# Kernel optimization log

Hardware: AMD Instinct MI355X
Metric: run time of the kernel (lower is better)

## Reference

```python
import jax, jax.numpy as jnp
import numpy as np

N_NODES = 20000
N_EDGES = 40000
MAX_NB = 6
N_ATOM_FEAT = 98
N_BOND_FEAT = 13
HIDDEN = 256
DEPTH = 4
INPUT_SIZE = N_ATOM_FEAT + N_BOND_FEAT  # 111, hmess width


def setup_inputs() -> dict:
    key = jax.random.key(0)
    ks = jax.random.split(key, 10)
    fnode = jax.random.normal(ks[0], (N_NODES, N_ATOM_FEAT), jnp.float32)
    # fmess: col0/col1 are src/dst node indices stored as floats, cols 2: are bond features
    idx = jax.random.randint(ks[1], (N_EDGES, 2), 0, N_NODES).astype(jnp.float32)
    bond = jax.random.normal(ks[2], (N_EDGES, N_BOND_FEAT), jnp.float32)
    fmess = jnp.concatenate([idx, bond], axis=1)  # [E, 2 + n_bond_feat]
    agraph = jax.random.randint(ks[3], (N_NODES, MAX_NB), 0, N_EDGES)
    bgraph = jax.random.randint(ks[4], (N_EDGES, MAX_NB), 0, N_EDGES)
    s = 0.02
    W_z_w = jax.random.normal(ks[5], (HIDDEN, INPUT_SIZE + HIDDEN), jnp.float32) * s
    W_z_b = jnp.zeros((HIDDEN,), jnp.float32)
    W_r_w = jax.random.normal(ks[6], (HIDDEN, INPUT_SIZE), jnp.float32) * s  # no bias (W_r)
    U_r_w = jax.random.normal(ks[7], (HIDDEN, HIDDEN), jnp.float32) * s
    U_r_b = jnp.zeros((HIDDEN,), jnp.float32)
    W_h_w = jax.random.normal(ks[8], (HIDDEN, INPUT_SIZE + HIDDEN), jnp.float32) * s
    W_h_b = jnp.zeros((HIDDEN,), jnp.float32)
    W_o_w = jax.random.normal(ks[9], (HIDDEN, N_ATOM_FEAT + HIDDEN), jnp.float32) * s
    W_o_b = jnp.zeros((HIDDEN,), jnp.float32)
    return dict(fnode=fnode, fmess=fmess, agraph=agraph, bgraph=bgraph,
                W_z_w=W_z_w, W_z_b=W_z_b, W_r_w=W_r_w, U_r_w=U_r_w, U_r_b=U_r_b,
                W_h_w=W_h_w, W_h_b=W_h_b, W_o_w=W_o_w, W_o_b=W_o_b)


def reference(fnode, fmess, agraph, bgraph,
              W_z_w, W_z_b, W_r_w, U_r_w, U_r_b, W_h_w, W_h_b, W_o_w, W_o_b):
    # GraphFeatEncoder: gather src-node features and concat with bond features
    src = fmess[:, 0].astype(jnp.int32)
    x = jnp.concatenate([fnode[src], fmess[:, 2:]], axis=-1)  # [E, input_size]
    E = x.shape[0]
    H = W_z_b.shape[0]
    emask = jnp.ones((E, 1), x.dtype).at[0, 0].set(0.0)  # message 0 is padding
    Wr_x = (x @ W_r_w.T)[:, None, :]  # [E,1,H], constant across depth iterations
    h = jnp.zeros((E, H), x.dtype)
    # DGCNGRU: D-MPNN style GRU over directed-edge states
    for _ in range(DEPTH):
        h_nei = h[bgraph]                                   # [E, max_nb, H] gather
        sum_h = h_nei.sum(axis=1)                           # [E, H]
        z = jax.nn.sigmoid(jnp.concatenate([x, sum_h], axis=1) @ W_z_w.T + W_z_b)
        r = jax.nn.sigmoid(Wr_x + h_nei @ U_r_w.T + U_r_b)  # [E, max_nb, H]
        sum_gh = (r * h_nei).sum(axis=1)
        pre_h = jnp.tanh(jnp.concatenate([x, sum_gh], axis=1) @ W_h_w.T + W_h_b)
        h = ((1.0 - z) * sum_h + z * pre_h) * emask
    # DGCNEncoder readout: aggregate incoming edge states per atom
    nei_msg = h[agraph].sum(axis=1)                          # [N, H] gather + sum
    node_h = jax.nn.gelu(jnp.concatenate([fnode, nei_msg], axis=1) @ W_o_w.T + W_o_b,
                         approximate=False)                  # torch nn.GELU = exact erf
    nmask = jnp.ones((node_h.shape[0], 1), node_h.dtype).at[0, 0].set(0.0)  # node 0 pad
    hatom = node_h * nmask
    return hatom  # GraphFeatEncoder returns (hatom, None); hmol is always None
```

## Files before the change

kernel.cpp:

```cpp
#include <hip/hip_runtime.h>
#include <cstddef>
#include <cstdint>

typedef unsigned short u16;
typedef unsigned int   u32;
typedef __bf16  bf16x8 __attribute__((ext_vector_type(8)));
typedef float   f32x4  __attribute__((ext_vector_type(4)));

#define DEV __device__ __forceinline__

DEV float b2f(u16 u) { union { u32 i; float f; } c; c.i = ((u32)u) << 16; return c.f; }
DEV u16 f2b(float x) { union { float f; u32 i; } c; c.f = x; u32 b = c.i;
                       return (u16)((b + 0x7FFFu + ((b >> 16) & 1u)) >> 16); }
DEV float sigm(float x)  { return 1.0f / (1.0f + __expf(-x)); }
DEV float tanh_(float x) { return 1.0f - 2.0f / (1.0f + __expf(2.0f * x)); }
DEV float gelu_(float x) { return 0.5f * x * (1.0f + erff(x * 0.70710678118654752f)); }

DEV void u4tof8(uint4 v, float* f) {
    f[0] = b2f((u16)(v.x & 0xFFFF)); f[1] = b2f((u16)(v.x >> 16));
    f[2] = b2f((u16)(v.y & 0xFFFF)); f[3] = b2f((u16)(v.y >> 16));
    f[4] = b2f((u16)(v.z & 0xFFFF)); f[5] = b2f((u16)(v.z >> 16));
    f[6] = b2f((u16)(v.w & 0xFFFF)); f[7] = b2f((u16)(v.w >> 16));
}
DEV uint4 f8tou4(const float* f) {
    uint4 v;
    v.x = (u32)f2b(f[0]) | ((u32)f2b(f[1]) << 16);
    v.y = (u32)f2b(f[2]) | ((u32)f2b(f[3]) << 16);
    v.z = (u32)f2b(f[4]) | ((u32)f2b(f[5]) << 16);
    v.w = (u32)f2b(f[6]) | ((u32)f2b(f[7]) << 16);
    return v;
}

#define OB_X     0ull
#define OB_FB    10240000ull
#define OB_PRU   15360000ull
#define OB_H     35840000ull
#define OB_UH    56320000ull
#define OB_SH    76800000ull
#define OB_SGH   97280000ull
#define OB_BZ    117760000ull
#define OB_BH    117956608ull
#define OB_BU    118153216ull
#define OB_BR    118284288ull
#define OB_BO    118349824ull
#define WS_BYTES 118546432ull


__global__ __launch_bounds__(256) void k_repack(
    const float* __restrict__ Wz, const float* __restrict__ Wr,
    const float* __restrict__ Ur, const float* __restrict__ Wh,
    const float* __restrict__ Wo,
    u16* __restrict__ BzT, u16* __restrict__ BhT, u16* __restrict__ BuT,
    u16* __restrict__ BrT, u16* __restrict__ BoT) {
    int idx = blockIdx.x * 256 + threadIdx.x;
    {
        int n = idx / 384, k = idx % 384;
        float vz, vh, vo;
        if (k < 111)      { vz = Wz[n * 367 + k];      vh = Wh[n * 367 + k]; }
        else if (k < 128) { vz = 0.0f;                 vh = 0.0f; }
        else              { vz = Wz[n * 367 + k - 17]; vh = Wh[n * 367 + k - 17]; }
        if (k < 98)       vo = Wo[n * 354 + k];
        else if (k < 128) vo = 0.0f;
        else              vo = Wo[n * 354 + k - 30];
        BzT[idx] = f2b(vz); BhT[idx] = f2b(vh); BoT[idx] = f2b(vo);
    }
    if (idx < 65536) BuT[idx] = f2b(Ur[idx]);
    if (idx < 32768) {
        int n = idx >> 7, k = idx & 127;
        BrT[idx] = f2b(k < 111 ? Wr[n * 111 + k] : 0.0f);
    }
}

__global__ __launch_bounds__(256) void k_build_x(const float* __restrict__ fnode,
                                                 const float* __restrict__ fmess,
                                                 u16* __restrict__ x) {
    int e = (blockIdx.x << 1) + (threadIdx.x >> 7);
    int c = threadIdx.x & 127;
    int src = (int)fmess[(size_t)e * 15];
    float v = 0.0f;
    if (c < 98)       v = fnode[(size_t)src * 98 + c];
    else if (c < 111) v = fmess[(size_t)e * 15 + 2 + (c - 98)];
    x[(size_t)e * 128 + c] = f2b(v);
}

__global__ __launch_bounds__(256) void k_build_fb(const float* __restrict__ fnode,
                                                  u16* __restrict__ fb) {
    int idx = blockIdx.x * 256 + threadIdx.x;
    int n = idx >> 7, c = idx & 127;
    fb[idx] = f2b(c < 98 ? fnode[(size_t)n * 98 + c] : 0.0f);
}

DEV void ldA(const u16* __restrict__ g, size_t row0, int ld, int k0, int tid, uint4* v) {
    #pragma unroll
    for (int it = 0; it < 4; ++it) {
        int r = it * 32 + (tid >> 3);
        int c = (tid & 7) << 3;
        v[it] = *(const uint4*)(g + (row0 + (size_t)r) * ld + k0 + c);
    }
}
DEV void ldB(const u16* __restrict__ g, size_t row0, int ld, int k0, int tid, uint4* v) {
    #pragma unroll
    for (int it = 0; it < 2; ++it) {
        int r = it * 32 + (tid >> 3);
        int c = (tid & 7) << 3;
        v[it] = *(const uint4*)(g + (row0 + (size_t)r) * ld + k0 + c);
    }
}
DEV void wrA(u16* s, int tid, const uint4* v) {
    #pragma unroll
    for (int it = 0; it < 4; ++it) {
        int r = it * 32 + (tid >> 3);
        int c = (tid & 7) << 3;
        int byte = (((r << 6) + c) << 1) ^ ((r & 7) << 4);
        *(uint4*)((char*)s + byte) = v[it];
    }
}
DEV void wrB(u16* s, int tid, const uint4* v) {
    #pragma unroll
    for (int it = 0; it < 2; ++it) {
        int r = it * 32 + (tid >> 3);
        int c = (tid & 7) << 3;
        int byte = (((r << 6) + c) << 1) ^ ((r & 7) << 4);
        *(uint4*)((char*)s + byte) = v[it];
    }
}
DEV void mma_step(const u16* As, const u16* Bs, f32x4 acc[4][2], int lane, int wr, int wc) {
    int rb = (wr << 6) + (lane & 15);
    int cb = (wc << 5) + (lane & 15);
    int ko = (lane >> 4) << 3;
    #pragma unroll
    for (int kh = 0; kh < 2; ++kh) {
        bf16x8 a[4], b[2];
        #pragma unroll
        for (int i = 0; i < 4; ++i) {
            int ar = rb + (i << 4);
            a[i] = *(const bf16x8*)((const char*)As +
                   ((((ar << 6) + (kh << 5) + ko) << 1) ^ ((ar & 7) << 4)));
        }
        #pragma unroll
        for (int j = 0; j < 2; ++j) {
            int br = cb + (j << 4);
            b[j] = *(const bf16x8*)((const char*)Bs +
                   ((((br << 6) + (kh << 5) + ko) << 1) ^ ((br & 7) << 4)));
        }
        #pragma unroll
        for (int i = 0; i < 4; ++i)
            #pragma unroll
            for (int j = 0; j < 2; ++j)
                acc[i][j] = __builtin_amdgcn_mfma_f32_16x16x32_bf16(b[j], a[i], acc[i][j], 0, 0, 0);
    }
}

#define GT_PROLOG()                                            \
    int tid = threadIdx.x, lane = tid & 63, w = tid >> 6;      \
    int wr = w >> 1, wc = w & 1;                               \
    int bm = blockIdx.x >> 2, bn = blockIdx.x & 3;             \
    size_t m0 = (size_t)bm << 7; size_t n0 = (size_t)(bn << 6);\
    int row_l = (wr << 6) + (lane & 15);                       \
    int col_l = (wc << 5) + ((lane >> 4) << 2);

#define ACC_INIT(A)                                            \
    { f32x4 zz = {0.f, 0.f, 0.f, 0.f};                         \
      _Pragma("unroll") for (int i = 0; i < 4; ++i)            \
      _Pragma("unroll") for (int j = 0; j < 2; ++j) A[i][j] = zz; }

#define DB_STEP(CUR_A, CUR_B, NXT_A, NXT_B, LD_NEXT2)          \
    mma_step(CUR_A, CUR_B, acc, lane, wr, wc);                 \
    wrA(NXT_A, tid, ra); wrB(NXT_B, tid, rb);                  \
    __syncthreads();                                           \
    LD_NEXT2;

__global__ __launch_bounds__(256) void k_mg_z(
    const u16* __restrict__ x, const u16* __restrict__ sumh,
    const u16* __restrict__ BzT, const float* __restrict__ bz,
    u16* __restrict__ zb) {
    __shared__ u16 As0[8192], As1[8192], Bs0[4096], Bs1[4096];
    GT_PROLOG()
    f32x4 acc[4][2]; ACC_INIT(acc)
    uint4 ra[4], rb[2];
    ldA(x, m0, 128, 0, tid, ra); ldB(BzT, n0, 384, 0, tid, rb);
    wrA(As0, tid, ra); wrB(Bs0, tid, rb);
    __syncthreads();
    ldA(x, m0, 128, 64, tid, ra); ldB(BzT, n0, 384, 64, tid, rb);
    DB_STEP(As0, Bs0, As1, Bs1, (ldA(sumh, m0, 256, 0, tid, ra),   ldB(BzT, n0, 384, 128, tid, rb)))
    DB_STEP(As1, Bs1, As0, Bs0, (ldA(sumh, m0, 256, 64, tid, ra),  ldB(BzT, n0, 384, 192, tid, rb)))
    DB_STEP(As0, Bs0, As1, Bs1, (ldA(sumh, m0, 256, 128, tid, ra), ldB(BzT, n0, 384, 256, tid, rb)))
    DB_STEP(As1, Bs1, As0, Bs0, (ldA(sumh, m0, 256, 192, tid, ra), ldB(BzT, n0, 384, 320, tid, rb)))
    DB_STEP(As0, Bs0, As1, Bs1, ;)
    mma_step(As1, Bs1, acc, lane, wr, wc);
    #pragma unroll
    for (int mi = 0; mi < 4; ++mi) {
        int m = (int)m0 + row_l + (mi << 4);
        if (m >= 40000) continue;
        #pragma unroll
        for (int ni = 0; ni < 2; ++ni) {
            int col = (int)n0 + col_l + (ni << 4);
            float4 vz = *(const float4*)(bz + col);
            ushort4 o;
            o.x = f2b(sigm(acc[mi][ni][0] + vz.x));
            o.y = f2b(sigm(acc[mi][ni][1] + vz.y));
            o.z = f2b(sigm(acc[mi][ni][2] + vz.z));
            o.w = f2b(sigm(acc[mi][ni][3] + vz.w));
            *(ushort4*)(zb + (size_t)m * 256 + col) = o;
        }
    }
}

__global__ __launch_bounds__(256) void k_mg_h(
    const u16* __restrict__ x, const u16* __restrict__ sumgh,
    const u16* __restrict__ sumh, const u16* __restrict__ zb,
    const u16* __restrict__ BhT, const float* __restrict__ bh,
    u16* __restrict__ h) {
    __shared__ u16 As0[8192], As1[8192], Bs0[4096], Bs1[4096];
    GT_PROLOG()
    f32x4 acc[4][2]; ACC_INIT(acc)
    uint4 ra[4], rb[2];
    ldA(x, m0, 128, 0, tid, ra); ldB(BhT, n0, 384, 0, tid, rb);
    wrA(As0, tid, ra); wrB(Bs0, tid, rb);
    __syncthreads();
    ldA(x, m0, 128, 64, tid, ra); ldB(BhT, n0, 384, 64, tid, rb);
    DB_STEP(As0, Bs0, As1, Bs1, (ldA(sumgh, m0, 256, 0, tid, ra),   ldB(BhT, n0, 384, 128, tid, rb)))
    DB_STEP(As1, Bs1, As0, Bs0, (ldA(sumgh, m0, 256, 64, tid, ra),  ldB(BhT, n0, 384, 192, tid, rb)))
    DB_STEP(As0, Bs0, As1, Bs1, (ldA(sumgh, m0, 256, 128, tid, ra), ldB(BhT, n0, 384, 256, tid, rb)))
    DB_STEP(As1, Bs1, As0, Bs0, (ldA(sumgh, m0, 256, 192, tid, ra), ldB(BhT, n0, 384, 320, tid, rb)))
    DB_STEP(As0, Bs0, As1, Bs1, ;)
    mma_step(As1, Bs1, acc, lane, wr, wc);
    #pragma unroll
    for (int mi = 0; mi < 4; ++mi) {
        int m = (int)m0 + row_l + (mi << 4);
        if (m >= 40000) continue;
        #pragma unroll
        for (int ni = 0; ni < 2; ++ni) {
            int col = (int)n0 + col_l + (ni << 4);
            float4 vh = *(const float4*)(bh + col);
            ushort4 z4  = *(const ushort4*)(zb   + (size_t)m * 256 + col);
            ushort4 sh4 = *(const ushort4*)(sumh + (size_t)m * 256 + col);
            float zv[4]  = {b2f(z4.x),  b2f(z4.y),  b2f(z4.z),  b2f(z4.w)};
            float shv[4] = {b2f(sh4.x), b2f(sh4.y), b2f(sh4.z), b2f(sh4.w)};
            float bhv[4] = {vh.x, vh.y, vh.z, vh.w};
            float o[4];
            #pragma unroll
            for (int q = 0; q < 4; ++q) {
                float pre = tanh_(acc[mi][ni][q] + bhv[q]);
                o[q] = (1.0f - zv[q]) * shv[q] + zv[q] * pre;
            }
            if (m == 0) { o[0] = o[1] = o[2] = o[3] = 0.0f; }
            ushort4 ov;
            ov.x = f2b(o[0]); ov.y = f2b(o[1]); ov.z = f2b(o[2]); ov.w = f2b(o[3]);
            *(ushort4*)(h + (size_t)m * 256 + col) = ov;
        }
    }
}

__global__ __launch_bounds__(256) void k_d1z(
    const u16* __restrict__ x, const u16* __restrict__ BzT,
    const float* __restrict__ bz, u16* __restrict__ zb) {
    __shared__ u16 As0[8192], As1[8192], Bs0[4096], Bs1[4096];
    GT_PROLOG()
    f32x4 acc[4][2]; ACC_INIT(acc)
    uint4 ra[4], rb[2];
    ldA(x, m0, 128, 0, tid, ra); ldB(BzT, n0, 384, 0, tid, rb);
    wrA(As0, tid, ra); wrB(Bs0, tid, rb);
    __syncthreads();
    ldA(x, m0, 128, 64, tid, ra); ldB(BzT, n0, 384, 64, tid, rb);
    DB_STEP(As0, Bs0, As1, Bs1, ;)
    mma_step(As1, Bs1, acc, lane, wr, wc);
    #pragma unroll
    for (int mi = 0; mi < 4; ++mi) {
        int m = (int)m0 + row_l + (mi << 4);
        if (m >= 40000) continue;
        #pragma unroll
        for (int ni = 0; ni < 2; ++ni) {
            int col = (int)n0 + col_l + (ni << 4);
            float4 vz = *(const float4*)(bz + col);
            ushort4 o;
            o.x = f2b(sigm(acc[mi][ni][0] + vz.x));
            o.y = f2b(sigm(acc[mi][ni][1] + vz.y));
            o.z = f2b(sigm(acc[mi][ni][2] + vz.z));
            o.w = f2b(sigm(acc[mi][ni][3] + vz.w));
            *(ushort4*)(zb + (size_t)m * 256 + col) = o;
        }
    }
}

__global__ __launch_bounds__(256) void k_d1h(
    const u16* __restrict__ x, const u16* __restrict__ zb,
    const u16* __restrict__ BhT, const float* __restrict__ bh,
    u16* __restrict__ h) {
    __shared__ u16 As0[8192], As1[8192], Bs0[4096], Bs1[4096];
    GT_PROLOG()
    f32x4 acc[4][2]; ACC_INIT(acc)
    uint4 ra[4], rb[2];
    ldA(x, m0, 128, 0, tid, ra); ldB(BhT, n0, 384, 0, tid, rb);
    wrA(As0, tid, ra); wrB(Bs0, tid, rb);
    __syncthreads();
    ldA(x, m0, 128, 64, tid, ra); ldB(BhT, n0, 384, 64, tid, rb);
    DB_STEP(As0, Bs0, As1, Bs1, ;)
    mma_step(As1, Bs1, acc, lane, wr, wc);
    #pragma unroll
    for (int mi = 0; mi < 4; ++mi) {
        int m = (int)m0 + row_l + (mi << 4);
        if (m >= 40000) continue;
        #pragma unroll
        for (int ni = 0; ni < 2; ++ni) {
            int col = (int)n0 + col_l + (ni << 4);
            float4 vh = *(const float4*)(bh + col);
            ushort4 z4 = *(const ushort4*)(zb + (size_t)m * 256 + col);
            float zv[4] = {b2f(z4.x), b2f(z4.y), b2f(z4.z), b2f(z4.w)};
            float o[4];
            o[0] = zv[0] * tanh_(acc[mi][ni][0] + vh.x);
            o[1] = zv[1] * tanh_(acc[mi][ni][1] + vh.y);
            o[2] = zv[2] * tanh_(acc[mi][ni][2] + vh.z);
            o[3] = zv[3] * tanh_(acc[mi][ni][3] + vh.w);
            if (m == 0) { o[0] = o[1] = o[2] = o[3] = 0.0f; }
            ushort4 ov;
            ov.x = f2b(o[0]); ov.y = f2b(o[1]); ov.z = f2b(o[2]); ov.w = f2b(o[3]);
            *(ushort4*)(h + (size_t)m * 256 + col) = ov;
        }
    }
}

__global__ __launch_bounds__(256) void k_mg_uh(
    const u16* __restrict__ A, const u16* __restrict__ BT, u16* __restrict__ C) {
    __shared__ u16 As0[8192], As1[8192], Bs0[4096], Bs1[4096];
    GT_PROLOG()
    f32x4 acc[4][2]; ACC_INIT(acc)
    uint4 ra[4], rb[2];
    ldA(A, m0, 256, 0, tid, ra); ldB(BT, n0, 256, 0, tid, rb);
    wrA(As0, tid, ra); wrB(Bs0, tid, rb);
    __syncthreads();
    ldA(A, m0, 256, 64, tid, ra); ldB(BT, n0, 256, 64, tid, rb);
    DB_STEP(As0, Bs0, As1, Bs1, (ldA(A, m0, 256, 128, tid, ra), ldB(BT, n0, 256, 128, tid, rb)))
    DB_STEP(As1, Bs1, As0, Bs0, (ldA(A, m0, 256, 192, tid, ra), ldB(BT, n0, 256, 192, tid, rb)))
    DB_STEP(As0, Bs0, As1, Bs1, ;)
    mma_step(As1, Bs1, acc, lane, wr, wc);
    #pragma unroll
    for (int mi = 0; mi < 4; ++mi) {
        int m = (int)m0 + row_l + (mi << 4);
        if (m >= 40000) continue;
        #pragma unroll
        for (int ni = 0; ni < 2; ++ni) {
            int col = (int)n0 + col_l + (ni << 4);
            ushort4 o;
            o.x = f2b(acc[mi][ni][0]); o.y = f2b(acc[mi][ni][1]);
            o.z = f2b(acc[mi][ni][2]); o.w = f2b(acc[mi][ni][3]);
            *(ushort4*)(C + (size_t)m * 256 + col) = o;
        }
    }
}

__global__ __launch_bounds__(256) void k_mg_p(
    const u16* __restrict__ x, const u16* __restrict__ BrT,
    const float* __restrict__ urb, u16* __restrict__ PrU) {
    __shared__ u16 As0[8192], As1[8192], Bs0[4096], Bs1[4096];
    GT_PROLOG()
    f32x4 acc[4][2]; ACC_INIT(acc)
    uint4 ra[4], rb[2];
    ldA(x, m0, 128, 0, tid, ra); ldB(BrT, n0, 128, 0, tid, rb);
    wrA(As0, tid, ra); wrB(Bs0, tid, rb);
    __syncthreads();
    ldA(x, m0, 128, 64, tid, ra); ldB(BrT, n0, 128, 64, tid, rb);
    DB_STEP(As0, Bs0, As1, Bs1, ;)
    mma_step(As1, Bs1, acc, lane, wr, wc);
    #pragma unroll
    for (int mi = 0; mi < 4; ++mi) {
        int m = (int)m0 + row_l + (mi << 4);
        if (m >= 40000) continue;
        #pragma unroll
        for (int ni = 0; ni < 2; ++ni) {
            int col = (int)n0 + col_l + (ni << 4);
            float4 ub = *(const float4*)(urb + col);
            ushort4 o;
            o.x = f2b(acc[mi][ni][0] + ub.x); o.y = f2b(acc[mi][ni][1] + ub.y);
            o.z = f2b(acc[mi][ni][2] + ub.z); o.w = f2b(acc[mi][ni][3] + ub.w);
            *(ushort4*)(PrU + (size_t)m * 256 + col) = o;
        }
    }
}

__global__ __launch_bounds__(256) void k_mg_out(
    const u16* __restrict__ fb, const u16* __restrict__ nei,
    const u16* __restrict__ BoT, const float* __restrict__ bo,
    float* __restrict__ out) {
    __shared__ u16 As0[8192], As1[8192], Bs0[4096], Bs1[4096];
    GT_PROLOG()
    f32x4 acc[4][2]; ACC_INIT(acc)
    uint4 ra[4], rb[2];
    ldA(fb, m0, 128, 0, tid, ra); ldB(BoT, n0, 384, 0, tid, rb);
    wrA(As0, tid, ra); wrB(Bs0, tid, rb);
    __syncthreads();
    ldA(fb, m0, 128, 64, tid, ra); ldB(BoT, n0, 384, 64, tid, rb);
    DB_STEP(As0, Bs0, As1, Bs1, (ldA(nei, m0, 256, 0, tid, ra),   ldB(BoT, n0, 384, 128, tid, rb)))
    DB_STEP(As1, Bs1, As0, Bs0, (ldA(nei, m0, 256, 64, tid, ra),  ldB(BoT, n0, 384, 192, tid, rb)))
    DB_STEP(As0, Bs0, As1, Bs1, (ldA(nei, m0, 256, 128, tid, ra), ldB(BoT, n0, 384, 256, tid, rb)))
    DB_STEP(As1, Bs1, As0, Bs0, (ldA(nei, m0, 256, 192, tid, ra), ldB(BoT, n0, 384, 320, tid, rb)))
    DB_STEP(As0, Bs0, As1, Bs1, ;)
    mma_step(As1, Bs1, acc, lane, wr, wc);
    #pragma unroll
    for (int mi = 0; mi < 4; ++mi) {
        int m = (int)m0 + row_l + (mi << 4);
        if (m >= 20000) continue;
        #pragma unroll
        for (int ni = 0; ni < 2; ++ni) {
            int col = (int)n0 + col_l + (ni << 4);
            float4 vb = *(const float4*)(bo + col);
            float4 o;
            o.x = gelu_(acc[mi][ni][0] + vb.x);
            o.y = gelu_(acc[mi][ni][1] + vb.y);
            o.z = gelu_(acc[mi][ni][2] + vb.z);
            o.w = gelu_(acc[mi][ni][3] + vb.w);
            if (m == 0) { o.x = o.y = o.z = o.w = 0.0f; }
            *(float4*)(out + (size_t)m * 256 + col) = o;
        }
    }
}

__global__ __launch_bounds__(256) void k_gather_edge(
    const u16* __restrict__ h, const u16* __restrict__ Uh,
    const u16* __restrict__ PrU, const int* __restrict__ bgraph,
    u16* __restrict__ sumh, u16* __restrict__ sumgh) {
    int e = (blockIdx.x << 3) + (threadIdx.x >> 5);
    int c = (threadIdx.x & 31) << 3;
    size_t o = (size_t)e * 256 + c;
    float pr[8];
    u4tof8(*(const uint4*)(PrU + o), pr);
    float sh[8] = {}, sg[8] = {};
    #pragma unroll
    for (int j = 0; j < 6; ++j) {
        int b = bgraph[e * 6 + j];
        float hv[8], uv[8];
        u4tof8(*(const uint4*)(h  + (size_t)b * 256 + c), hv);
        u4tof8(*(const uint4*)(Uh + (size_t)b * 256 + c), uv);
        #pragma unroll
        for (int q = 0; q < 8; ++q) {
            sh[q] += hv[q];
            sg[q] += sigm(pr[q] + uv[q]) * hv[q];
        }
    }
    *(uint4*)(sumh  + o) = f8tou4(sh);
    *(uint4*)(sumgh + o) = f8tou4(sg);
}

__global__ __launch_bounds__(256) void k_gather_node(
    const u16* __restrict__ h, const int* __restrict__ agraph,
    u16* __restrict__ nei) {
    int n = (blockIdx.x << 3) + (threadIdx.x >> 5);
    int c = (threadIdx.x & 31) << 3;
    float s[8] = {};
    #pragma unroll
    for (int j = 0; j < 6; ++j) {
        int a = agraph[n * 6 + j];
        float hv[8];
        u4tof8(*(const uint4*)(h + (size_t)a * 256 + c), hv);
        #pragma unroll
        for (int q = 0; q < 8; ++q) s[q] += hv[q];
    }
    *(uint4*)(nei + (size_t)n * 256 + c) = f8tou4(s);
}

extern "C" void kernel_launch(void* const* d_in, const int* in_sizes, int n_in,
                              void* d_out, int out_size, void* d_ws, size_t ws_size,
                              hipStream_t stream) {
    if (ws_size < WS_BYTES) return;

    const float* fnode  = (const float*)d_in[0];
    const float* fmess  = (const float*)d_in[1];
    const int*   agraph = (const int*)d_in[2];
    const int*   bgraph = (const int*)d_in[3];
    const float* Wz  = (const float*)d_in[4];
    const float* bz  = (const float*)d_in[5];
    const float* Wr  = (const float*)d_in[6];
    const float* Ur  = (const float*)d_in[7];
    const float* urb = (const float*)d_in[8];
    const float* Wh  = (const float*)d_in[9];
    const float* bh  = (const float*)d_in[10];
    const float* Wo  = (const float*)d_in[11];
    const float* bo  = (const float*)d_in[12];

    char* base = (char*)d_ws;
    u16* x     = (u16*)(base + OB_X);
    u16* fb    = (u16*)(base + OB_FB);
    u16* PrU   = (u16*)(base + OB_PRU);
    u16* h     = (u16*)(base + OB_H);
    u16* Uh    = (u16*)(base + OB_UH);
    u16* zb    = (u16*)(base + OB_UH);
    u16* nei   = (u16*)(base + OB_UH);
    u16* sumh  = (u16*)(base + OB_SH);
    u16* sumgh = (u16*)(base + OB_SGH);
    u16* BzT   = (u16*)(base + OB_BZ);
    u16* BhT   = (u16*)(base + OB_BH);
    u16* BuT   = (u16*)(base + OB_BU);
    u16* BrT   = (u16*)(base + OB_BR);
    u16* BoT   = (u16*)(base + OB_BO);
    float* out = (float*)d_out;

    hipLaunchKernelGGL(k_repack, dim3(384), dim3(256), 0, stream,
                       Wz, Wr, Ur, Wh, Wo, BzT, BhT, BuT, BrT, BoT);
    hipLaunchKernelGGL(k_build_x, dim3(20000), dim3(256), 0, stream, fnode, fmess, x);
    hipLaunchKernelGGL(k_build_fb, dim3(10000), dim3(256), 0, stream, fnode, fb);
    hipLaunchKernelGGL(k_mg_p, dim3(1252), dim3(256), 0, stream, x, BrT, urb, PrU);
    hipLaunchKernelGGL(k_d1z, dim3(1252), dim3(256), 0, stream, x, BzT, bz, zb);
    hipLaunchKernelGGL(k_d1h, dim3(1252), dim3(256), 0, stream, x, zb, BhT, bh, h);
    for (int d = 1; d < 4; ++d) {
        hipLaunchKernelGGL(k_mg_uh, dim3(1252), dim3(256), 0, stream, h, BuT, Uh);
        hipLaunchKernelGGL(k_gather_edge, dim3(5000), dim3(256), 0, stream,
                           h, Uh, PrU, bgraph, sumh, sumgh);
        hipLaunchKernelGGL(k_mg_z, dim3(1252), dim3(256), 0, stream,
                           x, sumh, BzT, bz, zb);
        hipLaunchKernelGGL(k_mg_h, dim3(1252), dim3(256), 0, stream,
                           x, sumgh, sumh, zb, BhT, bh, h);
    }
    hipLaunchKernelGGL(k_gather_node, dim3(2500), dim3(256), 0, stream, h, agraph, nei);
    hipLaunchKernelGGL(k_mg_out, dim3(628), dim3(256), 0, stream, fb, nei, BoT, bo, out);
}
```

Before: 470.4 us.

## Precompute depth-invariant x projections and split GEMMs into x and hidden parts

The x-dependent parts of the z, h and output projections are computed once up front as Pzx, Phx and a partial output, so the per-depth z/h GEMMs only multiply the 256-wide hidden part (K drops from 384 to 256). The first depth becomes an elementwise kernel, and the output GEMM adds a precomputed fnode partial stored in out. Tiles are also remapped across XCDs, and the gather kernels prefetch their indices and neighbour rows one step ahead. This cuts repeated GEMM work per depth but adds extra bf16 intermediate buffers and rounding of the partial projections.

Result: faster. 444.1 us (-5.6%).

```diff
diff --git a/kernel.cpp b/kernel.cpp
--- a/kernel.cpp
+++ b/kernel.cpp
@@ -31,43 +31,51 @@
     return v;
 }
 
-#define OB_X     0ull
-#define OB_FB    10240000ull
-#define OB_PRU   15360000ull
-#define OB_H     35840000ull
-#define OB_UH    56320000ull
-#define OB_SH    76800000ull
-#define OB_SGH   97280000ull
-#define OB_BZ    117760000ull
-#define OB_BH    117956608ull
-#define OB_BU    118153216ull
-#define OB_BR    118284288ull
-#define OB_BO    118349824ull
-#define WS_BYTES 118546432ull
-
+#define OB_PRU   0ull
+#define OB_PZX   20480000ull
+#define OB_PHX   40960000ull
+#define OB_H     61440000ull
+#define OB_UH    81920000ull
+#define OB_SH    102400000ull
+#define OB_SGH   122880000ull
+#define OB_BZX   143360000ull
+#define OB_BZH   143425536ull
+#define OB_BHX   143556608ull
+#define OB_BHH   143622144ull
+#define OB_BU    143753216ull
+#define OB_BOH   143884288ull
+#define OB_BR    OB_UH
+#define OB_BOX   (OB_UH + 65536ull)
+#define WS_BYTES 144015360ull
+
+
+DEV int xcd_swz(int bid, int nwg) {
+    int q = nwg >> 3, r = nwg & 7;
+    int xcd = bid & 7, idx = bid >> 3;
+    return (xcd < r ? xcd * (q + 1) : r * (q + 1) + (xcd - r) * q) + idx;
+}
 
 __global__ __launch_bounds__(256) void k_repack(
     const float* __restrict__ Wz, const float* __restrict__ Wr,
     const float* __restrict__ Ur, const float* __restrict__ Wh,
     const float* __restrict__ Wo,
-    u16* __restrict__ BzT, u16* __restrict__ BhT, u16* __restrict__ BuT,
-    u16* __restrict__ BrT, u16* __restrict__ BoT) {
+    u16* __restrict__ BzxT, u16* __restrict__ BzhT, u16* __restrict__ BhxT,
+    u16* __restrict__ BhhT, u16* __restrict__ BuT, u16* __restrict__ BohT,
+    u16* __restrict__ BrT, u16* __restrict__ BoxT) {
     int idx = blockIdx.x * 256 + threadIdx.x;
     {
-        int n = idx / 384, k = idx % 384;
-        float vz, vh, vo;
-        if (k < 111)      { vz = Wz[n * 367 + k];      vh = Wh[n * 367 + k]; }
-        else if (k < 128) { vz = 0.0f;                 vh = 0.0f; }
-        else              { vz = Wz[n * 367 + k - 17]; vh = Wh[n * 367 + k - 17]; }
-        if (k < 98)       vo = Wo[n * 354 + k];
-        else if (k < 128) vo = 0.0f;
-        else              vo = Wo[n * 354 + k - 30];
-        BzT[idx] = f2b(vz); BhT[idx] = f2b(vh); BoT[idx] = f2b(vo);
-    }
-    if (idx < 65536) BuT[idx] = f2b(Ur[idx]);
+        int n = idx >> 8, k = idx & 255;
+        BzhT[idx] = f2b(Wz[n * 367 + 111 + k]);
+        BhhT[idx] = f2b(Wh[n * 367 + 111 + k]);
+        BuT[idx]  = f2b(Ur[idx]);
+        BohT[idx] = f2b(Wo[n * 354 + 98 + k]);
+    }
     if (idx < 32768) {
         int n = idx >> 7, k = idx & 127;
-        BrT[idx] = f2b(k < 111 ? Wr[n * 111 + k] : 0.0f);
+        BzxT[idx] = f2b(k < 111 ? Wz[n * 367 + k] : 0.0f);
+        BhxT[idx] = f2b(k < 111 ? Wh[n * 367 + k] : 0.0f);
+        BrT[idx]  = f2b(k < 111 ? Wr[n * 111 + k] : 0.0f);
+        BoxT[idx] = f2b(k < 98  ? Wo[n * 354 + k] : 0.0f);
     }
 }
 
@@ -154,7 +162,8 @@
 #define GT_PROLOG()                                            \
     int tid = threadIdx.x, lane = tid & 63, w = tid >> 6;      \
     int wr = w >> 1, wc = w & 1;                               \
-    int bm = blockIdx.x >> 2, bn = blockIdx.x & 3;             \
+    int bid = xcd_swz((int)blockIdx.x, (int)gridDim.x);        \
+    int bm = bid >> 2, bn = bid & 3;                           \
     size_t m0 = (size_t)bm << 7; size_t n0 = (size_t)(bn << 6);\
     int row_l = (wr << 6) + (lane & 15);                       \
     int col_l = (wc << 5) + ((lane >> 4) << 2);
@@ -170,22 +179,17 @@
     __syncthreads();                                           \
     LD_NEXT2;
 
-__global__ __launch_bounds__(256) void k_mg_z(
-    const u16* __restrict__ x, const u16* __restrict__ sumh,
-    const u16* __restrict__ BzT, const float* __restrict__ bz,
-    u16* __restrict__ zb) {
+__global__ __launch_bounds__(256) void k_mg_k128(
+    const u16* __restrict__ A, const u16* __restrict__ BT,
+    const float* __restrict__ bias, u16* __restrict__ out) {
     __shared__ u16 As0[8192], As1[8192], Bs0[4096], Bs1[4096];
     GT_PROLOG()
     f32x4 acc[4][2]; ACC_INIT(acc)
     uint4 ra[4], rb[2];
-    ldA(x, m0, 128, 0, tid, ra); ldB(BzT, n0, 384, 0, tid, rb);
+    ldA(A, m0, 128, 0, tid, ra); ldB(BT, n0, 128, 0, tid, rb);
     wrA(As0, tid, ra); wrB(Bs0, tid, rb);
     __syncthreads();
-    ldA(x, m0, 128, 64, tid, ra); ldB(BzT, n0, 384, 64, tid, rb);
-    DB_STEP(As0, Bs0, As1, Bs1, (ldA(sumh, m0, 256, 0, tid, ra),   ldB(BzT, n0, 384, 128, tid, rb)))
-    DB_STEP(As1, Bs1, As0, Bs0, (ldA(sumh, m0, 256, 64, tid, ra),  ldB(BzT, n0, 384, 192, tid, rb)))
-    DB_STEP(As0, Bs0, As1, Bs1, (ldA(sumh, m0, 256, 128, tid, ra), ldB(BzT, n0, 384, 256, tid, rb)))
-    DB_STEP(As1, Bs1, As0, Bs0, (ldA(sumh, m0, 256, 192, tid, ra), ldB(BzT, n0, 384, 320, tid, rb)))
+    ldA(A, m0, 128, 64, tid, ra); ldB(BT, n0, 128, 64, tid, rb);
     DB_STEP(As0, Bs0, As1, Bs1, ;)
     mma_step(As1, Bs1, acc, lane, wr, wc);
     #pragma unroll
@@ -195,129 +199,57 @@
         #pragma unroll
         for (int ni = 0; ni < 2; ++ni) {
             int col = (int)n0 + col_l + (ni << 4);
-            float4 vz = *(const float4*)(bz + col);
+            float4 ub = bias ? *(const float4*)(bias + col)
+                             : make_float4(0.f, 0.f, 0.f, 0.f);
             ushort4 o;
-            o.x = f2b(sigm(acc[mi][ni][0] + vz.x));
-            o.y = f2b(sigm(acc[mi][ni][1] + vz.y));
-            o.z = f2b(sigm(acc[mi][ni][2] + vz.z));
-            o.w = f2b(sigm(acc[mi][ni][3] + vz.w));
-            *(ushort4*)(zb + (size_t)m * 256 + col) = o;
-        }
-    }
-}
-
-__global__ __launch_bounds__(256) void k_mg_h(
-    const u16* __restrict__ x, const u16* __restrict__ sumgh,
-    const u16* __restrict__ sumh, const u16* __restrict__ zb,
-    const u16* __restrict__ BhT, const float* __restrict__ bh,
-    u16* __restrict__ h) {
+            o.x = f2b(acc[mi][ni][0] + ub.x); o.y = f2b(acc[mi][ni][1] + ub.y);
+            o.z = f2b(acc[mi][ni][2] + ub.z); o.w = f2b(acc[mi][ni][3] + ub.w);
+            *(ushort4*)(out + (size_t)m * 256 + col) = o;
+        }
+    }
+}
+
+__global__ __launch_bounds__(256) void k_mg_pn(
+    const u16* __restrict__ fb, const u16* __restrict__ BT,
+    float* __restrict__ out) {
     __shared__ u16 As0[8192], As1[8192], Bs0[4096], Bs1[4096];
     GT_PROLOG()
     f32x4 acc[4][2]; ACC_INIT(acc)
     uint4 ra[4], rb[2];
-    ldA(x, m0, 128, 0, tid, ra); ldB(BhT, n0, 384, 0, tid, rb);
+    ldA(fb, m0, 128, 0, tid, ra); ldB(BT, n0, 128, 0, tid, rb);
     wrA(As0, tid, ra); wrB(Bs0, tid, rb);
     __syncthreads();
-    ldA(x, m0, 128, 64, tid, ra); ldB(BhT, n0, 384, 64, tid, rb);
-    DB_STEP(As0, Bs0, As1, Bs1, (ldA(sumgh, m0, 256, 0, tid, ra),   ldB(BhT, n0, 384, 128, tid, rb)))
-    DB_STEP(As1, Bs1, As0, Bs0, (ldA(sumgh, m0, 256, 64, tid, ra),  ldB(BhT, n0, 384, 192, tid, rb)))
-    DB_STEP(As0, Bs0, As1, Bs1, (ldA(sumgh, m0, 256, 128, tid, ra), ldB(BhT, n0, 384, 256, tid, rb)))
-    DB_STEP(As1, Bs1, As0, Bs0, (ldA(sumgh, m0, 256, 192, tid, ra), ldB(BhT, n0, 384, 320, tid, rb)))
+    ldA(fb, m0, 128, 64, tid, ra); ldB(BT, n0, 128, 64, tid, rb);
     DB_STEP(As0, Bs0, As1, Bs1, ;)
     mma_step(As1, Bs1, acc, lane, wr, wc);
     #pragma unroll
     for (int mi = 0; mi < 4; ++mi) {
         int m = (int)m0 + row_l + (mi << 4);
-        if (m >= 40000) continue;
+        if (m >= 20000) continue;
         #pragma unroll
         for (int ni = 0; ni < 2; ++ni) {
             int col = (int)n0 + col_l + (ni << 4);
-            float4 vh = *(const float4*)(bh + col);
-            ushort4 z4  = *(const ushort4*)(zb   + (size_t)m * 256 + col);
-            ushort4 sh4 = *(const ushort4*)(sumh + (size_t)m * 256 + col);
-            float zv[4]  = {b2f(z4.x),  b2f(z4.y),  b2f(z4.z),  b2f(z4.w)};
-            float shv[4] = {b2f(sh4.x), b2f(sh4.y), b2f(sh4.z), b2f(sh4.w)};
-            float bhv[4] = {vh.x, vh.y, vh.z, vh.w};
-            float o[4];
             #pragma unroll
-            for (int q = 0; q < 4; ++q) {
-                float pre = tanh_(acc[mi][ni][q] + bhv[q]);
-                o[q] = (1.0f - zv[q]) * shv[q] + zv[q] * pre;
-            }
-            if (m == 0) { o[0] = o[1] = o[2] = o[3] = 0.0f; }
-            ushort4 ov;
-            ov.x = f2b(o[0]); ov.y = f2b(o[1]); ov.z = f2b(o[2]); ov.w = f2b(o[3]);
-            *(ushort4*)(h + (size_t)m * 256 + col) = ov;
-        }
-    }
-}
-
-__global__ __launch_bounds__(256) void k_d1z(
-    const u16* __restrict__ x, const u16* __restrict__ BzT,
-    const float* __restrict__ bz, u16* __restrict__ zb) {
-    __shared__ u16 As0[8192], As1[8192], Bs0[4096], Bs1[4096];
-    GT_PROLOG()
-    f32x4 acc[4][2]; ACC_INIT(acc)
-    uint4 ra[4], rb[2];
-    ldA(x, m0, 128, 0, tid, ra); ldB(BzT, n0, 384, 0, tid, rb);
-    wrA(As0, tid, ra); wrB(Bs0, tid, rb);
-    __syncthreads();
-    ldA(x, m0, 128, 64, tid, ra); ldB(BzT, n0, 384, 64, tid, rb);
-    DB_STEP(As0, Bs0, As1, Bs1, ;)
-    mma_step(As1, Bs1, acc, lane, wr, wc);
-    #pragma unroll
-    for (int mi = 0; mi < 4; ++mi) {
-        int m = (int)m0 + row_l + (mi << 4);
-        if (m >= 40000) continue;
-        #pragma unroll
-        for (int ni = 0; ni < 2; ++ni) {
-            int col = (int)n0 + col_l + (ni << 4);
-            float4 vz = *(const float4*)(bz + col);
-            ushort4 o;
-            o.x = f2b(sigm(acc[mi][ni][0] + vz.x));
-            o.y = f2b(sigm(acc[mi][ni][1] + vz.y));
-            o.z = f2b(sigm(acc[mi][ni][2] + vz.z));
-            o.w = f2b(sigm(acc[mi][ni][3] + vz.w));
-            *(ushort4*)(zb + (size_t)m * 256 + col) = o;
-        }
-    }
-}
-
-__global__ __launch_bounds__(256) void k_d1h(
-    const u16* __restrict__ x, const u16* __restrict__ zb,
-    const u16* __restrict__ BhT, const float* __restrict__ bh,
+            for (int q = 0; q < 4; ++q)
+                out[(size_t)m * 256 + col + q] = acc[mi][ni][q];
+        }
+    }
+}
+
+__global__ __launch_bounds__(256) void k_d1(
+    const u16* __restrict__ Pzx, const u16* __restrict__ Phx,
+    const float* __restrict__ bz, const float* __restrict__ bh,
     u16* __restrict__ h) {
-    __shared__ u16 As0[8192], As1[8192], Bs0[4096], Bs1[4096];
-    GT_PROLOG()
-    f32x4 acc[4][2]; ACC_INIT(acc)
-    uint4 ra[4], rb[2];
-    ldA(x, m0, 128, 0, tid, ra); ldB(BhT, n0, 384, 0, tid, rb);
-    wrA(As0, tid, ra); wrB(Bs0, tid, rb);
-    __syncthreads();
-    ldA(x, m0, 128, 64, tid, ra); ldB(BhT, n0, 384, 64, tid, rb);
-    DB_STEP(As0, Bs0, As1, Bs1, ;)
-    mma_step(As1, Bs1, acc, lane, wr, wc);
-    #pragma unroll
-    for (int mi = 0; mi < 4; ++mi) {
-        int m = (int)m0 + row_l + (mi << 4);
-        if (m >= 40000) continue;
-        #pragma unroll
-        for (int ni = 0; ni < 2; ++ni) {
-            int col = (int)n0 + col_l + (ni << 4);
-            float4 vh = *(const float4*)(bh + col);
-            ushort4 z4 = *(const ushort4*)(zb + (size_t)m * 256 + col);
-            float zv[4] = {b2f(z4.x), b2f(z4.y), b2f(z4.z), b2f(z4.w)};
-            float o[4];
-            o[0] = zv[0] * tanh_(acc[mi][ni][0] + vh.x);
-            o[1] = zv[1] * tanh_(acc[mi][ni][1] + vh.y);
-            o[2] = zv[2] * tanh_(acc[mi][ni][2] + vh.z);
-            o[3] = zv[3] * tanh_(acc[mi][ni][3] + vh.w);
-            if (m == 0) { o[0] = o[1] = o[2] = o[3] = 0.0f; }
-            ushort4 ov;
-            ov.x = f2b(o[0]); ov.y = f2b(o[1]); ov.z = f2b(o[2]); ov.w = f2b(o[3]);
-            *(ushort4*)(h + (size_t)m * 256 + col) = ov;
-        }
-    }
+    int idx = blockIdx.x * 256 + threadIdx.x;
+    int e = idx >> 5, c = (idx & 31) << 3;
+    size_t o = (size_t)e * 256 + c;
+    float pz[8], ph[8], r[8];
+    u4tof8(*(const uint4*)(Pzx + o), pz);
+    u4tof8(*(const uint4*)(Phx + o), ph);
+    #pragma unroll
+    for (int q = 0; q < 8; ++q)
+        r[q] = (e == 0) ? 0.0f : sigm(pz[q] + bz[c + q]) * tanh_(ph[q] + bh[c + q]);
+    *(uint4*)(h + o) = f8tou4(r);
 }
 
 __global__ __launch_bounds__(256) void k_mg_uh(
@@ -349,17 +281,20 @@
     }
 }
 
-__global__ __launch_bounds__(256) void k_mg_p(
-    const u16* __restrict__ x, const u16* __restrict__ BrT,
-    const float* __restrict__ urb, u16* __restrict__ PrU) {
+__global__ __launch_bounds__(256) void k_mg_z(
+    const u16* __restrict__ sumh, const u16* __restrict__ BT,
+    const u16* __restrict__ Pzx, const float* __restrict__ bz,
+    u16* __restrict__ zb) {
     __shared__ u16 As0[8192], As1[8192], Bs0[4096], Bs1[4096];
     GT_PROLOG()
     f32x4 acc[4][2]; ACC_INIT(acc)
     uint4 ra[4], rb[2];
-    ldA(x, m0, 128, 0, tid, ra); ldB(BrT, n0, 128, 0, tid, rb);
+    ldA(sumh, m0, 256, 0, tid, ra); ldB(BT, n0, 256, 0, tid, rb);
     wrA(As0, tid, ra); wrB(Bs0, tid, rb);
     __syncthreads();
-    ldA(x, m0, 128, 64, tid, ra); ldB(BrT, n0, 128, 64, tid, rb);
+    ldA(sumh, m0, 256, 64, tid, ra); ldB(BT, n0, 256, 64, tid, rb);
+    DB_STEP(As0, Bs0, As1, Bs1, (ldA(sumh, m0, 256, 128, tid, ra), ldB(BT, n0, 256, 128, tid, rb)))
+    DB_STEP(As1, Bs1, As0, Bs0, (ldA(sumh, m0, 256, 192, tid, ra), ldB(BT, n0, 256, 192, tid, rb)))
     DB_STEP(As0, Bs0, As1, Bs1, ;)
     mma_step(As1, Bs1, acc, lane, wr, wc);
     #pragma unroll
@@ -369,31 +304,77 @@
         #pragma unroll
         for (int ni = 0; ni < 2; ++ni) {
             int col = (int)n0 + col_l + (ni << 4);
-            float4 ub = *(const float4*)(urb + col);
+            float4 vz = *(const float4*)(bz + col);
+            ushort4 p4 = *(const ushort4*)(Pzx + (size_t)m * 256 + col);
             ushort4 o;
-            o.x = f2b(acc[mi][ni][0] + ub.x); o.y = f2b(acc[mi][ni][1] + ub.y);
-            o.z = f2b(acc[mi][ni][2] + ub.z); o.w = f2b(acc[mi][ni][3] + ub.w);
-            *(ushort4*)(PrU + (size_t)m * 256 + col) = o;
-        }
-    }
-}
-
-__global__ __launch_bounds__(256) void k_mg_out(
-    const u16* __restrict__ fb, const u16* __restrict__ nei,
-    const u16* __restrict__ BoT, const float* __restrict__ bo,
-    float* __restrict__ out) {
+            o.x = f2b(sigm(acc[mi][ni][0] + b2f(p4.x) + vz.x));
+            o.y = f2b(sigm(acc[mi][ni][1] + b2f(p4.y) + vz.y));
+            o.z = f2b(sigm(acc[mi][ni][2] + b2f(p4.z) + vz.z));
+            o.w = f2b(sigm(acc[mi][ni][3] + b2f(p4.w) + vz.w));
+            *(ushort4*)(zb + (size_t)m * 256 + col) = o;
+        }
+    }
+}
+
+__global__ __launch_bounds__(256) void k_mg_h(
+    const u16* __restrict__ sumgh, const u16* __restrict__ BT,
+    const u16* __restrict__ Phx, const float* __restrict__ bh,
+    const u16* __restrict__ zb, const u16* __restrict__ sumh,
+    u16* __restrict__ h) {
     __shared__ u16 As0[8192], As1[8192], Bs0[4096], Bs1[4096];
     GT_PROLOG()
     f32x4 acc[4][2]; ACC_INIT(acc)
     uint4 ra[4], rb[2];
-    ldA(fb, m0, 128, 0, tid, ra); ldB(BoT, n0, 384, 0, tid, rb);
+    ldA(sumgh, m0, 256, 0, tid, ra); ldB(BT, n0, 256, 0, tid, rb);
     wrA(As0, tid, ra); wrB(Bs0, tid, rb);
     __syncthreads();
-    ldA(fb, m0, 128, 64, tid, ra); ldB(BoT, n0, 384, 64, tid, rb);
-    DB_STEP(As0, Bs0, As1, Bs1, (ldA(nei, m0, 256, 0, tid, ra),   ldB(BoT, n0, 384, 128, tid, rb)))
-    DB_STEP(As1, Bs1, As0, Bs0, (ldA(nei, m0, 256, 64, tid, ra),  ldB(BoT, n0, 384, 192, tid, rb)))
-    DB_STEP(As0, Bs0, As1, Bs1, (ldA(nei, m0, 256, 128, tid, ra), ldB(BoT, n0, 384, 256, tid, rb)))
-    DB_STEP(As1, Bs1, As0, Bs0, (ldA(nei, m0, 256, 192, tid, ra), ldB(BoT, n0, 384, 320, tid, rb)))
+    ldA(sumgh, m0, 256, 64, tid, ra); ldB(BT, n0, 256, 64, tid, rb);
+    DB_STEP(As0, Bs0, As1, Bs1, (ldA(sumgh, m0, 256, 128, tid, ra), ldB(BT, n0, 256, 128, tid, rb)))
+    DB_STEP(As1, Bs1, As0, Bs0, (ldA(sumgh, m0, 256, 192, tid, ra), ldB(BT, n0, 256, 192, tid, rb)))
+    DB_STEP(As0, Bs0, As1, Bs1, ;)
+    mma_step(As1, Bs1, acc, lane, wr, wc);
+    #pragma unroll
+    for (int mi = 0; mi < 4; ++mi) {
+        int m = (int)m0 + row_l + (mi << 4);
+        if (m >= 40000) continue;
+        #pragma unroll
+        for (int ni = 0; ni < 2; ++ni) {
+            int col = (int)n0 + col_l + (ni << 4);
+            float4 vh = *(const float4*)(bh + col);
+            ushort4 p4  = *(const ushort4*)(Phx  + (size_t)m * 256 + col);
+            ushort4 z4  = *(const ushort4*)(zb   + (size_t)m * 256 + col);
+            ushort4 sh4 = *(const ushort4*)(sumh + (size_t)m * 256 + col);
+            float pv[4]  = {b2f(p4.x),  b2f(p4.y),  b2f(p4.z),  b2f(p4.w)};
+            float zv[4]  = {b2f(z4.x),  b2f(z4.y),  b2f(z4.z),  b2f(z4.w)};
+            float shv[4] = {b2f(sh4.x), b2f(sh4.y), b2f(sh4.z), b2f(sh4.w)};
+            float bhv[4] = {vh.x, vh.y, vh.z, vh.w};
+            float o[4];
+            #pragma unroll
+            for (int q = 0; q < 4; ++q) {
+                float pre = tanh_(acc[mi][ni][q] + pv[q] + bhv[q]);
+                o[q] = (1.0f - zv[q]) * shv[q] + zv[q] * pre;
+            }
+            if (m == 0) { o[0] = o[1] = o[2] = o[3] = 0.0f; }
+            ushort4 ov;
+            ov.x = f2b(o[0]); ov.y = f2b(o[1]); ov.z = f2b(o[2]); ov.w = f2b(o[3]);
+            *(ushort4*)(h + (size_t)m * 256 + col) = ov;
+        }
+    }
+}
+
+__global__ __launch_bounds__(256) void k_mg_out(
+    const u16* __restrict__ nei, const u16* __restrict__ BT,
+    const float* __restrict__ bo, float* __restrict__ out) {
+    __shared__ u16 As0[8192], As1[8192], Bs0[4096], Bs1[4096];
+    GT_PROLOG()
+    f32x4 acc[4][2]; ACC_INIT(acc)
+    uint4 ra[4], rb[2];
+    ldA(nei, m0, 256, 0, tid, ra); ldB(BT, n0, 256, 0, tid, rb);
+    wrA(As0, tid, ra); wrB(Bs0, tid, rb);
+    __syncthreads();
+    ldA(nei, m0, 256, 64, tid, ra); ldB(BT, n0, 256, 64, tid, rb);
+    DB_STEP(As0, Bs0, As1, Bs1, (ldA(nei, m0, 256, 128, tid, ra), ldB(BT, n0, 256, 128, tid, rb)))
+    DB_STEP(As1, Bs1, As0, Bs0, (ldA(nei, m0, 256, 192, tid, ra), ldB(BT, n0, 256, 192, tid, rb)))
     DB_STEP(As0, Bs0, As1, Bs1, ;)
     mma_step(As1, Bs1, acc, lane, wr, wc);
     #pragma unroll
@@ -404,13 +385,16 @@
         for (int ni = 0; ni < 2; ++ni) {
             int col = (int)n0 + col_l + (ni << 4);
             float4 vb = *(const float4*)(bo + col);
-            float4 o;
-            o.x = gelu_(acc[mi][ni][0] + vb.x);
-            o.y = gelu_(acc[mi][ni][1] + vb.y);
-            o.z = gelu_(acc[mi][ni][2] + vb.z);
-            o.w = gelu_(acc[mi][ni][3] + vb.w);
-            if (m == 0) { o.x = o.y = o.z = o.w = 0.0f; }
-            *(float4*)(out + (size_t)m * 256 + col) = o;
+            const float bv[4] = {vb.x, vb.y, vb.z, vb.w};
+            float o[4];
+            #pragma unroll
+            for (int q = 0; q < 4; ++q) {
+                float pn = out[(size_t)m * 256 + col + q];
+                o[q] = (m == 0) ? 0.0f : gelu_(acc[mi][ni][q] + pn + bv[q]);
+            }
+            #pragma unroll
+            for (int q = 0; q < 4; ++q)
+                out[(size_t)m * 256 + col + q] = o[q];
         }
     }
 }
@@ -422,20 +406,30 @@
     int e = (blockIdx.x << 3) + (threadIdx.x >> 5);
     int c = (threadIdx.x & 31) << 3;
     size_t o = (size_t)e * 256 + c;
+    int bi[6];
+    *(int2*)&bi[0] = *(const int2*)(bgraph + e * 6 + 0);
+    *(int2*)&bi[2] = *(const int2*)(bgraph + e * 6 + 2);
+    *(int2*)&bi[4] = *(const int2*)(bgraph + e * 6 + 4);
     float pr[8];
     u4tof8(*(const uint4*)(PrU + o), pr);
     float sh[8] = {}, sg[8] = {};
+    uint4 hv4 = *(const uint4*)(h  + (size_t)bi[0] * 256 + c);
+    uint4 uv4 = *(const uint4*)(Uh + (size_t)bi[0] * 256 + c);
     #pragma unroll
     for (int j = 0; j < 6; ++j) {
-        int b = bgraph[e * 6 + j];
+        uint4 hn, un;
+        if (j < 5) {
+            hn = *(const uint4*)(h  + (size_t)bi[j + 1] * 256 + c);
+            un = *(const uint4*)(Uh + (size_t)bi[j + 1] * 256 + c);
+        }
         float hv[8], uv[8];
-        u4tof8(*(const uint4*)(h  + (size_t)b * 256 + c), hv);
-        u4tof8(*(const uint4*)(Uh + (size_t)b * 256 + c), uv);
+        u4tof8(hv4, hv); u4tof8(uv4, uv);
         #pragma unroll
         for (int q = 0; q < 8; ++q) {
             sh[q] += hv[q];
             sg[q] += sigm(pr[q] + uv[q]) * hv[q];
         }
+        hv4 = hn; uv4 = un;
     }
     *(uint4*)(sumh  + o) = f8tou4(sh);
     *(uint4*)(sumgh + o) = f8tou4(sg);
@@ -446,14 +440,21 @@
     u16* __restrict__ nei) {
     int n = (blockIdx.x << 3) + (threadIdx.x >> 5);
     int c = (threadIdx.x & 31) << 3;
+    int ai[6];
+    *(int2*)&ai[0] = *(const int2*)(agraph + n * 6 + 0);
+    *(int2*)&ai[2] = *(const int2*)(agraph + n * 6 + 2);
+    *(int2*)&ai[4] = *(const int2*)(agraph + n * 6 + 4);
     float s[8] = {};
+    uint4 hv4 = *(const uint4*)(h + (size_t)ai[0] * 256 + c);
     #pragma unroll
     for (int j = 0; j < 6; ++j) {
-        int a = agraph[n * 6 + j];
+        uint4 hn;
+        if (j < 5) hn = *(const uint4*)(h + (size_t)ai[j + 1] * 256 + c);
         float hv[8];
-        u4tof8(*(const uint4*)(h + (size_t)a * 256 + c), hv);
+        u4tof8(hv4, hv);
         #pragma unroll
         for (int q = 0; q < 8; ++q) s[q] += hv[q];
+        hv4 = hn;
     }
     *(uint4*)(nei + (size_t)n * 256 + c) = f8tou4(s);
 }
@@ -478,38 +479,45 @@
     const float* bo  = (const float*)d_in[12];
 
     char* base = (char*)d_ws;
-    u16* x     = (u16*)(base + OB_X);
-    u16* fb    = (u16*)(base + OB_FB);
     u16* PrU   = (u16*)(base + OB_PRU);
+    u16* Pzx   = (u16*)(base + OB_PZX);
+    u16* Phx   = (u16*)(base + OB_PHX);
     u16* h     = (u16*)(base + OB_H);
     u16* Uh    = (u16*)(base + OB_UH);
     u16* zb    = (u16*)(base + OB_UH);
     u16* nei   = (u16*)(base + OB_UH);
     u16* sumh  = (u16*)(base + OB_SH);
+    u16* x     = (u16*)(base + OB_SH);
     u16* sumgh = (u16*)(base + OB_SGH);
-    u16* BzT   = (u16*)(base + OB_BZ);
-    u16* BhT   = (u16*)(base + OB_BH);
+    u16* fb    = (u16*)(base + OB_SGH);
+    u16* BzxT  = (u16*)(base + OB_BZX);
+    u16* BzhT  = (u16*)(base + OB_BZH);
+    u16* BhxT  = (u16*)(base + OB_BHX);
+    u16* BhhT  = (u16*)(base + OB_BHH);
     u16* BuT   = (u16*)(base + OB_BU);
+    u16* BohT  = (u16*)(base + OB_BOH);
     u16* BrT   = (u16*)(base + OB_BR);
-    u16* BoT   = (u16*)(base + OB_BO);
+    u16* BoxT  = (u16*)(base + OB_BOX);
     float* out = (float*)d_out;
 
-    hipLaunchKernelGGL(k_repack, dim3(384), dim3(256), 0, stream,
-                       Wz, Wr, Ur, Wh, Wo, BzT, BhT, BuT, BrT, BoT);
+    hipLaunchKernelGGL(k_repack, dim3(256), dim3(256), 0, stream,
+                       Wz, Wr, Ur, Wh, Wo, BzxT, BzhT, BhxT, BhhT, BuT, BohT, BrT, BoxT);
     hipLaunchKernelGGL(k_build_x, dim3(20000), dim3(256), 0, stream, fnode, fmess, x);
     hipLaunchKernelGGL(k_build_fb, dim3(10000), dim3(256), 0, stream, fnode, fb);
-    hipLaunchKernelGGL(k_mg_p, dim3(1252), dim3(256), 0, stream, x, BrT, urb, PrU);
-    hipLaunchKernelGGL(k_d1z, dim3(1252), dim3(256), 0, stream, x, BzT, bz, zb);
-    hipLaunchKernelGGL(k_d1h, dim3(1252), dim3(256), 0, stream, x, zb, BhT, bh, h);
+    hipLaunchKernelGGL(k_mg_k128, dim3(1252), dim3(256), 0, stream, x, BrT, urb, PrU);
+    hipLaunchKernelGGL(k_mg_k128, dim3(1252), dim3(256), 0, stream, x, BzxT, (const float*)0, Pzx);
+    hipLaunchKernelGGL(k_mg_k128, dim3(1252), dim3(256), 0, stream, x, BhxT, (const float*)0, Phx);
+    hipLaunchKernelGGL(k_mg_pn, dim3(628), dim3(256), 0, stream, fb, BoxT, out);
+    hipLaunchKernelGGL(k_d1, dim3(5000), dim3(256), 0, stream, Pzx, Phx, bz, bh, h);
     for (int d = 1; d < 4; ++d) {
         hipLaunchKernelGGL(k_mg_uh, dim3(1252), dim3(256), 0, stream, h, BuT, Uh);
         hipLaunchKernelGGL(k_gather_edge, dim3(5000), dim3(256), 0, stream,
                            h, Uh, PrU, bgraph, sumh, sumgh);
         hipLaunchKernelGGL(k_mg_z, dim3(1252), dim3(256), 0, stream,
-                           x, sumh, BzT, bz, zb);
+                           sumh, BzhT, Pzx, bz, zb);
         hipLaunchKernelGGL(k_mg_h, dim3(1252), dim3(256), 0, stream,
-                           x, sumgh, sumh, zb, BhT, bh, h);
+                           sumgh, BhhT, Phx, bh, zb, sumh, h);
     }
     hipLaunchKernelGGL(k_gather_node, dim3(2500), dim3(256), 0, stream, h, agraph, nei);
-    hipLaunchKernelGGL(k_mg_out, dim3(628), dim3(256), 0, stream, fb, nei, BoT, bo, out);
-}
+    hipLaunchKernelGGL(k_mg_out, dim3(628), dim3(256), 0, stream, nei, BohT, bo, out);
+}
```
